# Performance work log

Measured on AMD Instinct MI355X. Metric: run time of the kernel, lower is better.

The kernel has to match this reference:

```python
import jax, jax.numpy as jnp
import numpy as np

NUM_BLOCKS = 6
D_MODEL = 1024
D_FF = 4096
NUM_HEADS = 16
NIN = 32
SEQ = NIN + 1  # +1 for SOS/EOS slot in the order-respecting mask
BATCH = 1024
D_HEAD = D_MODEL // NUM_HEADS
NEG = 1e10


def _order_masks(n):
    # order_respecting_mask with natural ordering arange(n)
    m0 = np.zeros((n + 1, n + 1), np.int32)  # input-layer mask
    m0[:, 0] = 1
    for s in range(n):
        for d in range(s + 1, n):
            m0[d, s + 1] = 1
    m0[-1, :] = 0
    mr = np.zeros((n + 1, n + 1), np.int32)  # later-layer mask (sees self)
    for s in range(n):
        for d in range(s, n):
            mr[d, s] = 1
    return jnp.asarray(m0), jnp.asarray(mr)


def setup_inputs() -> dict:
    key = jax.random.key(0)
    ks = jax.random.split(key, 6)
    std = 0.02  # Conv1d init std
    L, D, F = NUM_BLOCKS, D_MODEL, D_FF
    m0, mr = _order_masks(NIN)
    return {
        "x": jax.random.normal(ks[0], (BATCH, SEQ, D), jnp.float32),
        "qkv_w": std * jax.random.normal(ks[1], (L, D, 3 * D), jnp.float32),
        "qkv_b": jnp.zeros((L, 3 * D), jnp.float32),
        "proj_w": std * jax.random.normal(ks[2], (L, D, D), jnp.float32),
        "proj_b": jnp.zeros((L, D), jnp.float32),
        "w1": std * jax.random.normal(ks[3], (L, D, F), jnp.float32),
        "b1": jnp.zeros((L, F), jnp.float32),
        "w2": std * jax.random.normal(ks[4], (L, F, D), jnp.float32),
        "b2": jnp.zeros((L, D), jnp.float32),
        "ln1_s": jnp.ones((L, D), jnp.float32),
        "ln1_b": jnp.zeros((L, D), jnp.float32),
        "ln2_s": jnp.ones((L, D), jnp.float32),
        "ln2_b": jnp.zeros((L, D), jnp.float32),
        "lnf_s": jnp.ones((D,), jnp.float32),
        "lnf_b": jnp.zeros((D,), jnp.float32),
        "mask0": m0,
        "mask_rest": mr,
    }


def _ln(h, scale, shift, eps=1e-5):
    mean = h.mean(-1, keepdims=True)
    var = jnp.mean((h - mean) ** 2, axis=-1, keepdims=True)
    return scale * ((h - mean) * jax.lax.rsqrt(var + eps)) + shift


def _forward(x, qkv_w, qkv_b, proj_w, proj_b, w1, b1, w2, b2,
             ln1_s, ln1_b, ln2_s, ln2_b, lnf_s, lnf_b, mask0, mask_rest):
    B, S, D = x.shape
    H, Dh = NUM_HEADS, D_HEAD
    inv_sqrt_dk = 1.0 / np.sqrt(Dh).astype(np.float32)
    for l in range(qkv_w.shape[0]):
        m = (mask0 if l == 0 else mask_rest).astype(x.dtype)  # [S,S]
        h = _ln(x, ln1_s[l], ln1_b[l])
        qkv = h @ qkv_w[l] + qkv_b[l]  # [B,S,3D]
        q, k, v = [t.reshape(B, S, H, Dh) for t in jnp.split(qkv, 3, axis=-1)]
        scores = jnp.einsum('bshd,bthd->bhst', q, k) * inv_sqrt_dk  # [B,H,S,S]
        scores = scores * m - (1.0 - m) * NEG  # multiplicative+additive mask, as in source
        attn = jax.nn.softmax(scores, axis=-1)
        o = jnp.einsum('bhst,bthd->bshd', attn, v).reshape(B, S, D)
        x = x + (o @ proj_w[l] + proj_b[l])  # residual
        h = _ln(x, ln2_s[l], ln2_b[l])
        x = x + (jax.nn.gelu(h @ w1[l] + b1[l], approximate=False) @ w2[l] + b2[l])
    return _ln(x, lnf_s, lnf_b)  # ln_output=True


def reference(x, qkv_w, qkv_b, proj_w, proj_b, w1, b1, w2, b2,
              ln1_s, ln1_b, ln2_s, ln2_b, lnf_s, lnf_b, mask0, mask_rest):
    return _forward(x, qkv_w, qkv_b, proj_w, proj_b, w1, b1, w2, b2,
                    ln1_s, ln1_b, ln2_s, ln2_b, lnf_s, lnf_b, mask0, mask_rest)
```

## Files before the change

### kernel.cpp

```cpp
#include <hip/hip_runtime.h>

typedef unsigned short u16;
typedef __attribute__((ext_vector_type(8))) short s16x8;
typedef __attribute__((ext_vector_type(4))) float f32x4;

__device__ __forceinline__ float b2f(u16 u){ union{unsigned int i; float f;} v; v.i=((unsigned int)u)<<16; return v.f; }
__device__ __forceinline__ u16 f2b(float f){ union{float f; unsigned int i;} v; v.f=f; unsigned int r=v.i+0x7FFFu+((v.i>>16)&1u); return (u16)(r>>16); }

__device__ __forceinline__ void gload16(const void* g, void* l){
  __builtin_amdgcn_global_load_lds((const __attribute__((address_space(1))) void*)g,
                                   (__attribute__((address_space(3))) void*)l, 16, 0, 0);
}

__global__ void probe_k(const unsigned int* __restrict__ w, int* __restrict__ flag){
  if (threadIdx.x==0 && blockIdx.x==0) flag[0] = (w[0]!=0x3F800000u) ? 1 : 0;
}

__global__ __launch_bounds__(256) void conv2f32_k(const void* __restrict__ src, float* __restrict__ dst,
                                                  int n, const int* __restrict__ flag){
  const bool isb = flag[0]!=0;
  int i = (blockIdx.x*256+threadIdx.x)*4;
  for (int e=0;e<4;e++){
    int j=i+e;
    if (j<n) dst[j] = isb ? b2f(((const u16*)src)[j]) : ((const float*)src)[j];
  }
}

__global__ __launch_bounds__(256) void conv2bf16_k(const void* __restrict__ src, u16* __restrict__ dst,
                                                   int n, const int* __restrict__ flag){
  const bool isb = flag[0]!=0;
  int i = (blockIdx.x*256+threadIdx.x)*4;
  for (int e=0;e<4;e++){
    int j=i+e;
    if (j<n) dst[j] = isb ? ((const u16*)src)[j] : f2b(((const float*)src)[j]);
  }
}

__global__ __launch_bounds__(256) void transconv_k(const void* __restrict__ W, size_t ebase,
                                                   u16* __restrict__ Wt, int K, int Nc,
                                                   const int* __restrict__ flag){
  __shared__ float t[32][33];
  const bool isb = flag[0]!=0;
  const int n0 = blockIdx.x*32, k0 = blockIdx.y*32;
  const int tx = threadIdx.x, ty = threadIdx.y;
  #pragma unroll
  for (int r=0;r<4;r++){
    int row = ty + r*8;
    size_t idx = ebase + (size_t)(k0+row)*Nc + n0 + tx;
    t[row][tx] = isb ? b2f(((const u16*)W)[idx]) : ((const float*)W)[idx];
  }
  __syncthreads();
  #pragma unroll
  for (int r=0;r<4;r++){
    int row = ty + r*8;
    Wt[(size_t)(n0+row)*K + k0 + tx] = f2b(t[tx][row]);
  }
}

template<int XF32>
__global__ __launch_bounds__(256) void ln_k(const void* __restrict__ Xv, const float* __restrict__ sc,
                                            const float* __restrict__ sh, u16* __restrict__ O){
  const size_t t = blockIdx.x;
  const int tid = threadIdx.x;
  float x0,x1,x2,x3;
  if (XF32){
    float4 f = ((const float4*)Xv)[t*256 + tid];
    x0=f.x; x1=f.y; x2=f.z; x3=f.w;
  } else {
    uint2 u = *(const uint2*)((const u16*)Xv + t*1024 + tid*4);
    x0=b2f((u16)(u.x&0xFFFF)); x1=b2f((u16)(u.x>>16)); x2=b2f((u16)(u.y&0xFFFF)); x3=b2f((u16)(u.y>>16));
  }
  float s = x0+x1+x2+x3;
  float q = x0*x0+x1*x1+x2*x2+x3*x3;
  #pragma unroll
  for (int off=32; off; off>>=1){ s += __shfl_xor(s, off, 64); q += __shfl_xor(q, off, 64); }
  __shared__ float as[4], aq[4];
  if ((tid&63)==0){ as[tid>>6]=s; aq[tid>>6]=q; }
  __syncthreads();
  s = as[0]+as[1]+as[2]+as[3];
  q = aq[0]+aq[1]+aq[2]+aq[3];
  float mean = s*(1.0f/1024.0f);
  float var  = q*(1.0f/1024.0f) - mean*mean;
  float rs = rsqrtf(var + 1e-5f);
  int c = tid*4;
  float y0 = sc[c+0]*((x0-mean)*rs)+sh[c+0];
  float y1 = sc[c+1]*((x1-mean)*rs)+sh[c+1];
  float y2 = sc[c+2]*((x2-mean)*rs)+sh[c+2];
  float y3 = sc[c+3]*((x3-mean)*rs)+sh[c+3];
  uint2 o; o.x=(unsigned)f2b(y0)|((unsigned)f2b(y1)<<16); o.y=(unsigned)f2b(y2)|((unsigned)f2b(y3)<<16);
  *(uint2*)(O + t*1024 + tid*4) = o;
}

template<int XF32>
__global__ __launch_bounds__(256) void ln_out_k(const void* __restrict__ Xv, const float* __restrict__ sc,
                                                const float* __restrict__ sh, void* __restrict__ out,
                                                const int* __restrict__ flag){
  const size_t t = blockIdx.x;
  const int tid = threadIdx.x;
  float x0,x1,x2,x3;
  if (XF32){
    float4 f = ((const float4*)Xv)[t*256 + tid];
    x0=f.x; x1=f.y; x2=f.z; x3=f.w;
  } else {
    uint2 u = *(const uint2*)((const u16*)Xv + t*1024 + tid*4);
    x0=b2f((u16)(u.x&0xFFFF)); x1=b2f((u16)(u.x>>16)); x2=b2f((u16)(u.y&0xFFFF)); x3=b2f((u16)(u.y>>16));
  }
  float s = x0+x1+x2+x3;
  float q = x0*x0+x1*x1+x2*x2+x3*x3;
  #pragma unroll
  for (int off=32; off; off>>=1){ s += __shfl_xor(s, off, 64); q += __shfl_xor(q, off, 64); }
  __shared__ float as[4], aq[4];
  if ((tid&63)==0){ as[tid>>6]=s; aq[tid>>6]=q; }
  __syncthreads();
  s = as[0]+as[1]+as[2]+as[3];
  q = aq[0]+aq[1]+aq[2]+aq[3];
  float mean = s*(1.0f/1024.0f);
  float var  = q*(1.0f/1024.0f) - mean*mean;
  float rs = rsqrtf(var + 1e-5f);
  int c = tid*4;
  float y0 = sc[c+0]*((x0-mean)*rs)+sh[c+0];
  float y1 = sc[c+1]*((x1-mean)*rs)+sh[c+1];
  float y2 = sc[c+2]*((x2-mean)*rs)+sh[c+2];
  float y3 = sc[c+3]*((x3-mean)*rs)+sh[c+3];
  if (flag[0]){
    uint2 o; o.x=(unsigned)f2b(y0)|((unsigned)f2b(y1)<<16); o.y=(unsigned)f2b(y2)|((unsigned)f2b(y3)<<16);
    *(uint2*)((u16*)out + t*1024 + tid*4) = o;
  } else {
    float4 o4; o4.x=y0; o4.y=y1; o4.z=y2; o4.w=y3;
    ((float4*)out)[t*256 + tid] = o4;
  }
}

__global__ __launch_bounds__(128) void attn_k(const u16* __restrict__ QKV, const int* __restrict__ mask,
                                              u16* __restrict__ O){
  __shared__ float q[33][65];
  __shared__ float ks[33][65];
  __shared__ float vs[33][65];
  __shared__ float p[33][34];
  const int tid = threadIdx.x;
  const int b = blockIdx.x>>4, h = blockIdx.x&15;
  const size_t tok0 = (size_t)b*33;
  for (int idx=tid; idx<33*16; idx+=128){
    int s=idx>>4, d4=(idx&15)*4;
    size_t base=(tok0+s)*3072 + h*64 + d4;
    uint2 uq=*(const uint2*)(QKV+base);
    uint2 uk=*(const uint2*)(QKV+base+1024);
    uint2 uv=*(const uint2*)(QKV+base+2048);
    q[s][d4+0]=b2f((u16)(uq.x&0xFFFF)); q[s][d4+1]=b2f((u16)(uq.x>>16));
    q[s][d4+2]=b2f((u16)(uq.y&0xFFFF)); q[s][d4+3]=b2f((u16)(uq.y>>16));
    ks[s][d4+0]=b2f((u16)(uk.x&0xFFFF)); ks[s][d4+1]=b2f((u16)(uk.x>>16));
    ks[s][d4+2]=b2f((u16)(uk.y&0xFFFF)); ks[s][d4+3]=b2f((u16)(uk.y>>16));
    vs[s][d4+0]=b2f((u16)(uv.x&0xFFFF)); vs[s][d4+1]=b2f((u16)(uv.x>>16));
    vs[s][d4+2]=b2f((u16)(uv.y&0xFFFF)); vs[s][d4+3]=b2f((u16)(uv.y>>16));
  }
  __syncthreads();
  for (int idx=tid; idx<33*9; idx+=128){
    int s=idx/9, tg=idx-s*9;
    int t0=tg*4;
    float a0=0.f,a1=0.f,a2=0.f,a3=0.f;
    if (t0<=s && s<32){
      int t1=min(t0+1,32), t2=min(t0+2,32), t3=min(t0+3,32);
      #pragma unroll
      for (int d=0; d<64; d++){
        float qq=q[s][d];
        a0+=qq*ks[t0][d]; a1+=qq*ks[t1][d]; a2+=qq*ks[t2][d]; a3+=qq*ks[t3][d];
      }
    }
    float av[4]={a0,a1,a2,a3};
    #pragma unroll
    for (int e=0;e<4;e++){
      int t=t0+e;
      if (t<33) p[s][t] = mask[s*33+t] ? av[e]*0.125f : -1e10f;
    }
  }
  __syncthreads();
  if (tid<33){
    float mx=-3.4e38f;
    for (int t=0;t<33;t++) mx = fmaxf(mx, p[tid][t]);
    float sm=0.f;
    for (int t=0;t<33;t++){ float e=expf(p[tid][t]-mx); p[tid][t]=e; sm+=e; }
    float inv=1.0f/sm;
    for (int t=0;t<33;t++) p[tid][t]*=inv;
  }
  __syncthreads();
  for (int idx=tid; idx<33*16; idx+=128){
    int s=idx>>4, d4=(idx&15)*4;
    float a0=0.f,a1=0.f,a2=0.f,a3=0.f;
    for (int t=0;t<=s;t++){
      float pp=p[s][t];
      a0+=pp*vs[t][d4+0]; a1+=pp*vs[t][d4+1]; a2+=pp*vs[t][d4+2]; a3+=pp*vs[t][d4+3];
    }
    uint2 o; o.x=(unsigned)f2b(a0)|((unsigned)f2b(a1)<<16); o.y=(unsigned)f2b(a2)|((unsigned)f2b(a3)<<16);
    *(uint2*)(O + (tok0+s)*1024 + h*64 + d4) = o;
  }
}

template<int MODE>
__global__ __launch_bounds__(512,2) void gemm8_k(const u16* __restrict__ A, const u16* __restrict__ Bt,
                                                 const float* __restrict__ bias, void* __restrict__ Cv,
                                                 int Nc, int K){
  __shared__ u16 As[2][256*64];
  __shared__ u16 Bs[2][256*64];
  const int tid = threadIdx.x;
  const int wid = tid>>6, lane = tid&63;
  const int wmid = wid>>2, wnid = wid&3;
  const int r15 = lane&15, kg = lane>>4;

  const int gx = gridDim.x;
  int id = blockIdx.y*gx + blockIdx.x;
  const int nwg = gx*gridDim.y;
  const int q8 = nwg>>3, r8 = nwg&7;
  const int xcd = id&7; id >>= 3;
  const int nid = (xcd<r8 ? xcd*(q8+1) : r8*(q8+1)+(xcd-r8)*q8) + id;
  const int m0 = (nid/gx)*256, n0 = (nid%gx)*256;

  const int NT = K>>6;

  f32x4 acc[8][4];
  #pragma unroll
  for (int i=0;i<8;i++)
    #pragma unroll
    for (int j=0;j<4;j++) acc[i][j] = (f32x4){0.f,0.f,0.f,0.f};

  auto stageA = [&](int kt, int b, int h){
    #pragma unroll
    for (int i=0;i<2;i++){
      int c = h*1024 + i*512 + tid;
      int r = c>>3, cc = c&7;
      int gcc = cc ^ (r&7);
      gload16(A + (size_t)(m0+r)*K + (kt<<6) + gcc*8, &As[b][(size_t)c*8]);
    }
  };
  auto stageB = [&](int kt, int b, int h){
    #pragma unroll
    for (int i=0;i<2;i++){
      int c = h*1024 + i*512 + tid;
      int r = c>>3, cc = c&7;
      int gcc = cc ^ (r&7);
      gload16(Bt + (size_t)(n0+r)*K + (kt<<6) + gcc*8, &Bs[b][(size_t)c*8]);
    }
  };

  stageA(0,0,0); stageA(0,0,1); stageB(0,0,0); stageB(0,0,1);
  __syncthreads();

  int cur = 0;
  s16x8 bfr[4][2];
  for (int kt=0; kt<NT; ++kt){
    const bool pref = (kt+1 < NT);
    #pragma unroll
    for (int q=0;q<4;q++){
      if (q==0){
        #pragma unroll
        for (int j=0;j<4;j++){
          int row = wnid*64 + j*16 + r15;
          #pragma unroll
          for (int ks=0;ks<2;ks++)
            bfr[j][ks] = *(const s16x8*)(&Bs[cur][(size_t)row*64 + (((ks*4+kg)^(r15&7))<<3)]);
        }
      }
      s16x8 afr[2][2];
      #pragma unroll
      for (int ii=0;ii<2;ii++){
        int row = wmid*128 + (q*2+ii)*16 + r15;
        #pragma unroll
        for (int ks=0;ks<2;ks++)
          afr[ii][ks] = *(const s16x8*)(&As[cur][(size_t)row*64 + (((ks*4+kg)^(r15&7))<<3)]);
      }
      if (pref){
        if (q==0) stageA(kt+1, cur^1, 0);
        else if (q==1) stageA(kt+1, cur^1, 1);
        else if (q==2) stageB(kt+1, cur^1, 0);
        else stageB(kt+1, cur^1, 1);
      }
      __builtin_amdgcn_s_barrier();
      __builtin_amdgcn_s_setprio(1);
      #pragma unroll
      for (int ii=0;ii<2;ii++)
        #pragma unroll
        for (int j=0;j<4;j++)
          #pragma unroll
          for (int ks=0;ks<2;ks++)
            acc[q*2+ii][j] = __builtin_amdgcn_mfma_f32_16x16x32_bf16(afr[ii][ks], bfr[j][ks], acc[q*2+ii][j], 0, 0, 0);
      __builtin_amdgcn_s_setprio(0);
      if (q==3)
        asm volatile("s_waitcnt vmcnt(0)" ::: "memory");
      __builtin_amdgcn_s_barrier();
    }
    cur ^= 1;
  }

  #pragma unroll
  for (int i=0;i<8;i++){
    #pragma unroll
    for (int j=0;j<4;j++){
      int col = n0 + wnid*64 + j*16 + r15;
      float bc = bias[col];
      #pragma unroll
      for (int r=0;r<4;r++){
        int row = m0 + wmid*128 + i*16 + kg*4 + r;
        float vv = acc[i][j][r] + bc;
        if (MODE==1) vv = 0.5f*vv*(1.0f + erff(vv*0.70710678118f));
        size_t idx = (size_t)row*Nc + col;
        if (MODE==2){
          ((float*)Cv)[idx] += vv;
        } else if (MODE==3){
          u16* C = (u16*)Cv;
          C[idx] = f2b(vv + b2f(C[idx]));
        } else {
          ((u16*)Cv)[idx] = f2b(vv);
        }
      }
    }
  }
}

extern "C" void kernel_launch(void* const* d_in, const int* in_sizes, int n_in,
                              void* d_out, int out_size, void* d_ws, size_t ws_size,
                              hipStream_t stream){
  (void)in_sizes; (void)n_in; (void)out_size;
  const int L=6, D=1024, TD=3072, F=4096, NTOK=1024*33;
  const size_t PARAMN = 81920;

  auto need = [&](int xf32, int mc)->size_t{
    size_t t=0;
    auto add=[&](size_t b){ t=(t+255)&~(size_t)255; t+=b; };
    add((size_t)NTOK*D*(xf32?4:2)); add(PARAMN*4); add(4);
    add((size_t)mc*D*2); add((size_t)mc*F*2);
    add((size_t)TD*D*2); add((size_t)D*D*2); add((size_t)F*D*2); add((size_t)D*F*2);
    return t;
  };
  int xf32 = 1, mc = NTOK;
  if (ws_size < need(1,NTOK)){
    mc = 16896;
    if (ws_size < need(1,16896)){
      mc = 8448;
      if (ws_size < need(1,8448)) xf32 = 0;
    }
  }
  const int nch = NTOK/mc;

  char* basep = (char*)d_ws; size_t off=0;
  auto alloc=[&](size_t b)->char*{ off=(off+255)&~(size_t)255; char* p=basep+off; off+=b; return p; };
  void*  X   = (void*)alloc((size_t)NTOK*D*(xf32?4:2));
  float* pf  = (float*)alloc(PARAMN*4);
  int*   flag= (int*)alloc(4);
  u16*   H   = (u16*)alloc((size_t)mc*D*2);
  u16*   BIG = (u16*)alloc((size_t)mc*F*2);
  u16*   wQ  = (u16*)alloc((size_t)TD*D*2);
  u16*   wP  = (u16*)alloc((size_t)D*D*2);
  u16*   w1  = (u16*)alloc((size_t)F*D*2);
  u16*   w2  = (u16*)alloc((size_t)D*F*2);

  const size_t pQB=0, pPB=pQB+(size_t)L*TD, pB1=pPB+(size_t)L*D, pB2=pB1+(size_t)L*F,
               pL1S=pB2+(size_t)L*D, pL1B=pL1S+(size_t)L*D, pL2S=pL1B+(size_t)L*D,
               pL2B=pL2S+(size_t)L*D, pLFS=pL2B+(size_t)L*D, pLFB=pLFS+D;

  probe_k<<<1,64,0,stream>>>((const unsigned int*)d_in[9], flag);
  if (xf32) conv2f32_k<<<(NTOK*D)/1024,256,0,stream>>>(d_in[0], (float*)X, NTOK*D, flag);
  else      conv2bf16_k<<<(NTOK*D)/1024,256,0,stream>>>(d_in[0], (u16*)X, NTOK*D, flag);
  {
    struct PRM { int idx; size_t offe; int n; };
    const PRM prm[10] = {
      {2,pQB,L*TD},{4,pPB,L*D},{6,pB1,L*F},{8,pB2,L*D},
      {9,pL1S,L*D},{10,pL1B,L*D},{11,pL2S,L*D},{12,pL2B,L*D},
      {13,pLFS,D},{14,pLFB,D}};
    for (int i=0;i<10;i++)
      conv2f32_k<<<(prm[i].n+1023)/1024,256,0,stream>>>(d_in[prm[i].idx], pf+prm[i].offe, prm[i].n, flag);
  }

  const size_t xstride = (size_t)D*(xf32?4:2);
  for (int l=0;l<L;l++){
    transconv_k<<<dim3(TD/32, D/32), dim3(32,8),0,stream>>>(d_in[1], (size_t)l*D*TD, wQ, D, TD, flag);
    transconv_k<<<dim3(D/32,  D/32), dim3(32,8),0,stream>>>(d_in[3], (size_t)l*D*D,  wP, D, D,  flag);
    transconv_k<<<dim3(F/32,  D/32), dim3(32,8),0,stream>>>(d_in[5], (size_t)l*D*F,  w1, D, F,  flag);
    transconv_k<<<dim3(D/32,  F/32), dim3(32,8),0,stream>>>(d_in[7], (size_t)l*F*D,  w2, F, D,  flag);
    const int* msk = (const int*)d_in[l==0?15:16];
    for (int c=0;c<nch;c++){
      void* Xc = (void*)((char*)X + (size_t)c*mc*xstride);
      if (xf32) ln_k<1><<<mc,256,0,stream>>>(Xc, pf+pL1S+(size_t)l*D, pf+pL1B+(size_t)l*D, H);
      else      ln_k<0><<<mc,256,0,stream>>>(Xc, pf+pL1S+(size_t)l*D, pf+pL1B+(size_t)l*D, H);
      gemm8_k<0><<<dim3(TD/256, mc/256),512,0,stream>>>(H, wQ, pf+pQB+(size_t)l*TD, BIG, TD, D);
      attn_k<<<(mc/33)*16,128,0,stream>>>(BIG, msk, H);
      if (xf32) gemm8_k<2><<<dim3(D/256, mc/256),512,0,stream>>>(H, wP, pf+pPB+(size_t)l*D, Xc, D, D);
      else      gemm8_k<3><<<dim3(D/256, mc/256),512,0,stream>>>(H, wP, pf+pPB+(size_t)l*D, Xc, D, D);
      if (xf32) ln_k<1><<<mc,256,0,stream>>>(Xc, pf+pL2S+(size_t)l*D, pf+pL2B+(size_t)l*D, H);
      else      ln_k<0><<<mc,256,0,stream>>>(Xc, pf+pL2S+(size_t)l*D, pf+pL2B+(size_t)l*D, H);
      gemm8_k<1><<<dim3(F/256, mc/256),512,0,stream>>>(H, w1, pf+pB1+(size_t)l*F, BIG, F, D);
      if (xf32) gemm8_k<2><<<dim3(D/256, mc/256),512,0,stream>>>(BIG, w2, pf+pB2+(size_t)l*D, Xc, D, F);
      else      gemm8_k<3><<<dim3(D/256, mc/256),512,0,stream>>>(BIG, w2, pf+pB2+(size_t)l*D, Xc, D, F);
    }
  }
  if (xf32) ln_out_k<1><<<NTOK,256,0,stream>>>(X, pf+pLFS, pf+pLFB, d_out, flag);
  else      ln_out_k<0><<<NTOK,256,0,stream>>>(X, pf+pLFS, pf+pLFB, d_out, flag);
}
```

Measured before the change: 10.33 ms.

## Pipeline GEMM staging per quarter tile with fine-grained vmcnt waits

Reorganizes the bf16 GEMM's LDS staging so A and B tiles are loaded in quarter slices that match each compute phase. B slices for tile t+2 are prefetched into the buffer being consumed once its slice has been read, and counted vmcnt waits replace the single full drain at the end of each k-step. The aim is to keep global-to-LDS loads in flight continuously and avoid a full memory-wait bubble every iteration. The cost is intricate wait-count bookkeeping and reuse of buffers that are still live, which risks races if any count is wrong.

```diff
diff --git a/kernel.cpp b/kernel.cpp
--- a/kernel.cpp
+++ b/kernel.cpp
@@ -199,8 +199,8 @@
 __global__ __launch_bounds__(512,2) void gemm8_k(const u16* __restrict__ A, const u16* __restrict__ Bt,
                                                  const float* __restrict__ bias, void* __restrict__ Cv,
                                                  int Nc, int K){
-  __shared__ u16 As[2][256*64];
-  __shared__ u16 Bs[2][256*64];
+  __shared__ u16 As[2][16384];
+  __shared__ u16 Bs[2][16384];
   const int tid = threadIdx.x;
   const int wid = tid>>6, lane = tid&63;
   const int wmid = wid>>2, wnid = wid&3;
@@ -222,56 +222,67 @@
     #pragma unroll
     for (int j=0;j<4;j++) acc[i][j] = (f32x4){0.f,0.f,0.f,0.f};
 
-  auto stageA = [&](int kt, int b, int h){
-    #pragma unroll
-    for (int i=0;i<2;i++){
-      int c = h*1024 + i*512 + tid;
-      int r = c>>3, cc = c&7;
-      int gcc = cc ^ (r&7);
-      gload16(A + (size_t)(m0+r)*K + (kt<<6) + gcc*8, &As[b][(size_t)c*8]);
-    }
+  const int c_ = tid, rq_ = c_>>3, cc_ = c_&7;
+  const int gcc_ = cc_ ^ (rq_&7);
+  const int grA_ = (rq_<32) ? rq_ : (96 + rq_);
+
+  auto stageAq = [&](int kt, int b, int q){
+    gload16(A + (size_t)(m0 + q*32 + grA_)*K + (kt<<6) + gcc_*8, &As[b][q*4096 + c_*8]);
   };
-  auto stageB = [&](int kt, int b, int h){
-    #pragma unroll
-    for (int i=0;i<2;i++){
-      int c = h*1024 + i*512 + tid;
-      int r = c>>3, cc = c&7;
-      int gcc = cc ^ (r&7);
-      gload16(Bt + (size_t)(n0+r)*K + (kt<<6) + gcc*8, &Bs[b][(size_t)c*8]);
-    }
+  auto stageBq = [&](int kt, int b, int j){
+    gload16(Bt + (size_t)(n0 + j*64 + rq_)*K + (kt<<6) + gcc_*8, &Bs[b][j*4096 + c_*8]);
   };
 
-  stageA(0,0,0); stageA(0,0,1); stageB(0,0,0); stageB(0,0,1);
-  __syncthreads();
+  #pragma unroll
+  for (int q=0;q<4;q++) stageAq(0,0,q);
+  #pragma unroll
+  for (int q=0;q<4;q++) stageBq(0,0,q);
+  if (NT>1){ stageBq(1,1,0); stageBq(1,1,1); stageBq(1,1,2);
+    asm volatile("s_waitcnt vmcnt(3)" ::: "memory");
+  } else {
+    asm volatile("s_waitcnt vmcnt(0)" ::: "memory");
+  }
+  __builtin_amdgcn_s_barrier();
 
   int cur = 0;
   s16x8 bfr[4][2];
-  for (int kt=0; kt<NT; ++kt){
-    const bool pref = (kt+1 < NT);
+  for (int t=0; t<NT; ++t){
     #pragma unroll
     for (int q=0;q<4;q++){
+      if (t+2 < NT){
+        asm volatile("s_waitcnt vmcnt(6)" ::: "memory");
+      } else if (t+2 == NT){
+        if      (q<=1) asm volatile("s_waitcnt vmcnt(6)" ::: "memory");
+        else if (q==2) asm volatile("s_waitcnt vmcnt(5)" ::: "memory");
+        else           asm volatile("s_waitcnt vmcnt(4)" ::: "memory");
+      } else {
+        if      (q==0) asm volatile("s_waitcnt vmcnt(3)" ::: "memory");
+        else if (q==1) asm volatile("s_waitcnt vmcnt(2)" ::: "memory");
+        else if (q==2) asm volatile("s_waitcnt vmcnt(1)" ::: "memory");
+        else           asm volatile("s_waitcnt vmcnt(0)" ::: "memory");
+      }
+      s16x8 afr[2][2];
+      #pragma unroll
+      for (int ii=0;ii<2;ii++){
+        int rq = wmid*32 + ii*16 + r15;
+        #pragma unroll
+        for (int ks=0;ks<2;ks++)
+          afr[ii][ks] = *(const s16x8*)(&As[cur][q*4096 + rq*64 + (((ks*4+kg)^(rq&7))<<3)]);
+      }
       if (q==0){
         #pragma unroll
         for (int j=0;j<4;j++){
-          int row = wnid*64 + j*16 + r15;
+          int rq = j*16 + r15;
           #pragma unroll
           for (int ks=0;ks<2;ks++)
-            bfr[j][ks] = *(const s16x8*)(&Bs[cur][(size_t)row*64 + (((ks*4+kg)^(r15&7))<<3)]);
+            bfr[j][ks] = *(const s16x8*)(&Bs[cur][wnid*4096 + rq*64 + (((ks*4+kg)^(rq&7))<<3)]);
         }
       }
-      s16x8 afr[2][2];
-      #pragma unroll
-      for (int ii=0;ii<2;ii++){
-        int row = wmid*128 + (q*2+ii)*16 + r15;
-        #pragma unroll
-        for (int ks=0;ks<2;ks++)
-          afr[ii][ks] = *(const s16x8*)(&As[cur][(size_t)row*64 + (((ks*4+kg)^(r15&7))<<3)]);
-      }
-      if (pref){
-        if (q==0) stageA(kt+1, cur^1, 0);
-        else if (q==1) stageA(kt+1, cur^1, 1);
-        else if (q==2) stageB(kt+1, cur^1, 0);
-        else stageB(kt+1, cur^1, 1);
+      if (q==0){
+        if (t+1<NT){ stageAq(t+1, cur^1, 0); stageBq(t+1, cur^1, 3); }
+      } else {
+        if (t+1<NT) stageAq(t+1, cur^1, q);
+        if (t+2<NT) stageBq(t+2, cur, q-1);
       }
       __builtin_amdgcn_s_barrier();
       __builtin_amdgcn_s_setprio(1);
@@ -283,8 +294,6 @@
           for (int ks=0;ks<2;ks++)
             acc[q*2+ii][j] = __builtin_amdgcn_mfma_f32_16x16x32_bf16(afr[ii][ks], bfr[j][ks], acc[q*2+ii][j], 0, 0, 0);
       __builtin_amdgcn_s_setprio(0);
-      if (q==3)
-        asm volatile("s_waitcnt vmcnt(0)" ::: "memory");
       __builtin_amdgcn_s_barrier();
     }
     cur ^= 1;
```

Result: slower. 11.70 ms (+13.3%).
